# Optimization experiments

Hardware: AMD Instinct MI355X
Metric: run time of the kernel (lower is better)

## Reference

```python
import jax, jax.numpy as jnp
import numpy as np
import math

# static config (see shape_source)
NUM_GRAPHS = 8      # b
L_NODES = 1024      # nodes per graph (uniform -> to_dense_batch is a reshape)
D_INNER = 128
HEADDIM = 16
N_HEADS = D_INNER // HEADDIM  # 8
D_STATE = 64
NUM_DT = 4          # 3 node-dt components + dt_self
AVG_DEG = 16
DIAMETER = 50       # default_graph_diameter
TOL = 0.1
DT_MIN, DT_MAX, DT_FLOOR = 1e-3, 1e-1, 1e-4


def dag_inverse(A):
    """DAGInverse.forward: (I - A)^{-1} via repeated-squaring doubling.
    A: [b, h, l, l]. j = 2^ceil(log2(diameter)); out = prod (I + A^{2^k})."""
    j = 2 ** math.ceil(math.log2(DIAMETER))  # 64
    I = jnp.eye(A.shape[-1], dtype=A.dtype)
    last = A
    out = I + A
    for _ in range(2, int(math.log2(j)) + 1):  # 5 iterations
        last = last @ last
        out = out @ (I + last)
    return out


def setup_inputs() -> dict:
    key = jax.random.key(0)
    k = jax.random.split(key, 8)
    N = NUM_GRAPHS * L_NODES
    x = jax.random.normal(k[0], (N, D_INNER), jnp.float32)
    B_mat = jax.random.normal(k[1], (N, D_STATE), jnp.float32)
    C_mat = jax.random.normal(k[2], (N, D_STATE), jnp.float32)
    dt = jax.random.normal(k[3], (N, NUM_DT * N_HEADS), jnp.float32)
    # dt_bias init as in GraphSSD.__init__
    u = jax.random.uniform(k[4], (N_HEADS,), jnp.float32)
    dt0 = jnp.exp(u * (math.log(DT_MAX) - math.log(DT_MIN)) + math.log(DT_MIN))
    dt0 = jnp.clip(dt0, DT_FLOOR, None)
    dt_bias = dt0 + jnp.log(-jnp.expm1(-dt0))
    D = jnp.ones((N_HEADS,), jnp.float32)
    # edges: per-graph random endpoints, offset to global node ids
    E_per = L_NODES * AVG_DEG
    src_l = jax.random.randint(k[5], (NUM_GRAPHS, E_per), 0, L_NODES)
    dst_l = jax.random.randint(k[6], (NUM_GRAPHS, E_per), 0, L_NODES)
    off = (jnp.arange(NUM_GRAPHS) * L_NODES)[:, None]
    edge_index = jnp.stack([(src_l + off).reshape(-1), (dst_l + off).reshape(-1)], 0).astype(jnp.int32)
    return {"x": x, "B_mat": B_mat, "C_mat": C_mat, "dt": dt,
            "dt_bias": dt_bias, "D": D, "edge_index": edge_index}


def reference(x, B_mat, C_mat, dt, dt_bias, D, edge_index):
    Bn, Lg, H, hd, ds = NUM_GRAPHS, L_NODES, N_HEADS, HEADDIM, D_STATE
    N = Bn * Lg
    # dense batching (uniform graph sizes -> pure reshape, mask all True)
    x_d = x.reshape(Bn, Lg, H, hd).transpose(0, 2, 1, 3)        # b n l h ('(n h)' split)
    B_d = B_mat.reshape(Bn, Lg, ds)                             # broadcast over heads
    C_d = C_mat.reshape(Bn, Lg, ds)
    # dt: 'l (n c) -> c n l'
    dt_c = dt.reshape(N, H, NUM_DT).transpose(2, 1, 0)          # c n l
    dt_node, dt_self = dt_c[:NUM_DT - 1], dt_c[NUM_DT - 1]      # (3,n,N), (n,N)
    dt_self_d = dt_self.T.reshape(Bn, Lg, H).transpose(0, 2, 1)  # b n l
    # multiply_dt_w_A: A = -exp(A_log)= -1 (with_A=False)
    dt_A_node = -jax.nn.softplus(dt_node + dt_bias[None, :, None])  # (3, n, N)
    # edge dt: (dt_s[src] + dt_t[dst]) / 2, then exp
    src, dst = edge_index[0], edge_index[1]
    attr = jnp.exp((dt_A_node[0][:, src] + dt_A_node[1][:, dst]) * 0.5).T  # (E, n)
    # to_dense_adj scatter: [b, l1, l2, h] then -> b h l1 l2
    b_idx, sl, dl = src // Lg, src % Lg, dst % Lg
    A_mat = jnp.zeros((Bn, Lg, Lg, H), x.dtype).at[b_idx, sl, dl].add(attr)
    A_mat = A_mat.transpose(0, 3, 1, 2)                          # b n l1 l2
    # 'leq' normalization with dummy self term
    dt_dummy = jnp.exp(dt_A_node[2]).T.reshape(Bn, Lg, H).transpose(0, 2, 1)  # b n l
    normalizer = A_mat.sum(-1) + dt_dummy                        # b n l1
    A_norm = A_mat / (normalizer[..., None] + TOL)
    # L = (I - A^T)^{-1} via DAGInverse doubling
    Lmat = dag_inverse(jnp.swapaxes(A_norm, -1, -2).astype(jnp.float32))  # b n l t
    L_norm = Lmat * dt_self_d[:, :, None, :]                     # scale along t
    # y = einsum(C, L, B, x); C/B broadcast in heads -> G shared across heads
    G = jnp.einsum('bld,btd->blt', C_d, B_d)[:, None]            # b 1 l t
    y = jnp.einsum('bnlt,bnth->bnlh', L_norm * G, x_d)
    y = y + x_d * D[None, :, None, None]
    # 'b n l h -> b l (h n)'
    y = y.transpose(0, 2, 3, 1).reshape(Bn, Lg, H * hd)
    return y.reshape(N, H * hd)
```

## Files before the change

kernel.cpp:

```cpp
#include <hip/hip_runtime.h>
#include <hip/hip_bf16.h>

#define H_ 8
#define NTOT 8192
#define LG 1024
#define BN 8
#define HD 16
#define DSTATE 64
#define EPG 16384
#define MSZ (1024*1024)

typedef __hip_bfloat16 bf16;
typedef unsigned short ushort_t;
typedef _Float16 f16;
typedef __attribute__((ext_vector_type(8))) _Float16 half8;
typedef __attribute__((ext_vector_type(4))) _Float16 half4;
typedef __attribute__((ext_vector_type(4))) float f4v;

__device__ __forceinline__ float b2f(bf16 v){ return __bfloat162float(v); }
__device__ __forceinline__ float sp_(float z){
  return fmaxf(z, 0.f) + log1pf(expf(-fabsf(z)));
}
__device__ __forceinline__ float ldv(const void* p, size_t i, int f32){
  float v;
  if (f32) v = ((const float*)p)[i];
  else     v = b2f(((const bf16*)p)[i]);
  return v;
}
__device__ __forceinline__ void gl2lds16(const void* g, void* l){
  __builtin_amdgcn_global_load_lds((const __attribute__((address_space(1))) unsigned int*)g,
                                   (__attribute__((address_space(3))) unsigned int*)l,
                                   16, 0, 0);
}

__global__ void k_sniff(const void* __restrict__ dt, int* __restrict__ flag){
  const ushort_t* p = (const ushort_t*)dt;
  int tid = threadIdx.x;
  int bad = 0;
  for (int i = tid; i < 512; i += 256){
    int e = (p[i] >> 7) & 0xFF;
    if (e >= 140) bad = 1;
  }
  unsigned long long m = __ballot(bad != 0);
  __shared__ int anybad[4];
  if ((tid & 63) == 0) anybad[tid >> 6] = (m != 0ull) ? 1 : 0;
  __syncthreads();
  if (tid == 0) *flag = (anybad[0] | anybad[1] | anybad[2] | anybad[3]);
}

__global__ void k_nodecoef(const void* __restrict__ dt, const void* __restrict__ dtb,
                           const int* __restrict__ flag,
                           float* __restrict__ a0, float* __restrict__ a1,
                           float* __restrict__ dum, float* __restrict__ sdt){
  int idx = blockIdx.x*256 + threadIdx.x;
  if (idx >= H_*NTOT) return;
  int f32 = *flag;
  int h = idx / NTOT, n = idx - h*NTOT;
  float bias = ldv(dtb, h, f32);
  size_t base = (size_t)n*(4*H_) + h*4;
  float d0, d1, d2, d3;
  if (f32){
    const float* row = (const float*)dt + base;
    d0 = row[0]; d1 = row[1]; d2 = row[2]; d3 = row[3];
  } else {
    const bf16* row = (const bf16*)dt + base;
    d0 = b2f(row[0]); d1 = b2f(row[1]); d2 = b2f(row[2]); d3 = b2f(row[3]);
  }
  a0[idx]  = -sp_(d0 + bias);
  a1[idx]  = -sp_(d1 + bias);
  dum[idx] = expf(-sp_(d2 + bias));
  sdt[idx] = d3;
}

__global__ __launch_bounds__(256) void k_zero(char* base, size_t regB){
  int bh = blockIdx.y;
  float* Mf = (float*)(base + (size_t)bh*regB) + MSZ;
  int i = blockIdx.x*1024 + threadIdx.x*4;
  *(float4*)(Mf + i) = make_float4(0.f,0.f,0.f,0.f);
}

__global__ void k_scatter(const int* __restrict__ ei, const float* __restrict__ a0,
                          const float* __restrict__ a1, char* base, size_t regB,
                          float* __restrict__ nrm,
                          int b0, int h0, int lgHB, int GBp, int nthreads, int Etot){
  int t = blockIdx.x*256 + threadIdx.x;
  if (t >= nthreads) return;
  int HB = 1 << lgHB;
  int hl = t & (HB-1);
  int el = t >> lgHB;
  int e = b0*EPG + el;
  int src = ei[e], dst = ei[Etot + e];
  int g = src >> 10;
  if ((unsigned)(g - b0) >= (unsigned)GBp) return;
  int sl = src & 1023, dl = dst & 1023;
  int h = h0 + hl;
  float attr = expf(0.5f*(a0[h*NTOT + src] + a1[h*NTOT + dst]));
  int bhl = (g - b0)*HB + hl;
  float* Mf = (float*)(base + (size_t)bhl*regB) + MSZ;
  atomicAdd(&Mf[(size_t)dl*LG + sl], attr);
  atomicAdd(&nrm[bhl*LG + sl], attr);
}

__global__ void k_normalize(char* base, size_t regB,
                            const float* __restrict__ nrm, const float* __restrict__ dum,
                            int b0, int h0, int HB){
  size_t idx = (size_t)blockIdx.x*256 + threadIdx.x;
  int bh = (int)(idx >> 20);
  int rem = (int)(idx & (MSZ-1));
  int sl = rem & 1023, dl = rem >> 10;
  int g = b0 + bh / HB, h = h0 + bh % HB;
  const float* Mf = (const float*)(base + (size_t)bh*regB) + MSZ;
  f16* ub = (f16*)(base + (size_t)bh*regB);
  float denom = nrm[bh*LG + sl] + dum[h*NTOT + g*LG + sl] + 0.1f;
  float v = Mf[rem] / denom;
  ub[rem] = (f16)v;
  ub[(size_t)4*MSZ + rem] = (f16)(v + (dl == sl ? 1.f : 0.f));
}

__global__ __launch_bounds__(256) void k_transpose(char* base, size_t regB, int iS, int iD){
  __shared__ ushort_t t[32][33];
  int bh = blockIdx.z;
  const ushort_t* S = (const ushort_t*)(base + (size_t)bh*regB) + (size_t)iS*MSZ;
  ushort_t* D = (ushort_t*)(base + (size_t)bh*regB) + (size_t)iD*MSZ;
  int x0 = blockIdx.x*32, y0 = blockIdx.y*32;
  int tx = threadIdx.x & 31, ty = threadIdx.x >> 5;
  #pragma unroll
  for (int i = 0; i < 32; i += 8)
    t[ty+i][tx] = S[(size_t)(y0+ty+i)*LG + x0+tx];
  __syncthreads();
  #pragma unroll
  for (int i = 0; i < 32; i += 8)
    D[(size_t)(x0+ty+i)*LG + y0+tx] = t[tx][ty+i];
}

__global__ __launch_bounds__(256) void k_G(const void* __restrict__ Bm, const void* __restrict__ Cm,
                                           const int* __restrict__ flag,
                                           f16* __restrict__ G, int b0){
  int gl = blockIdx.z;
  int g = b0 + gl;
  int l0 = blockIdx.y*16, t0 = blockIdx.x*16;
  __shared__ float Cs[16][DSTATE+1];
  __shared__ float Bs[16][DSTATE+1];
  int tid = threadIdx.x;
  int f32 = *flag;
  if (f32){
    const float* Cf = (const float*)Cm;
    const float* Bf = (const float*)Bm;
    for (int i = tid; i < 16*DSTATE; i += 256){
      int r = i >> 6, d = i & 63;
      Cs[r][d] = Cf[(size_t)(g*LG + l0 + r)*DSTATE + d];
      Bs[r][d] = Bf[(size_t)(g*LG + t0 + r)*DSTATE + d];
    }
  } else {
    const bf16* Cb = (const bf16*)Cm;
    const bf16* Bb = (const bf16*)Bm;
    for (int i = tid; i < 16*DSTATE; i += 256){
      int r = i >> 6, d = i & 63;
      Cs[r][d] = b2f(Cb[(size_t)(g*LG + l0 + r)*DSTATE + d]);
      Bs[r][d] = b2f(Bb[(size_t)(g*LG + t0 + r)*DSTATE + d]);
    }
  }
  __syncthreads();
  int r = tid >> 4, c = tid & 15;
  float acc = 0.f;
  #pragma unroll
  for (int d = 0; d < DSTATE; ++d) acc = fmaf(Cs[r][d], Bs[c][d], acc);
  G[(size_t)gl*MSZ + (size_t)(l0+r)*LG + t0 + c] = (f16)acc;
}

__global__ __launch_bounds__(512, 6) void k_gemm_fused(char* base, size_t regB,
    int nS, int iAs, int iBTs, int iCs, int iCTs,
    int nU, int iAu, int iBTu, int iCu){
  __shared__ ushort_t As[2][4096];
  __shared__ ushort_t Bs[2][4096];
  int T = nS + nU;
  int s = blockIdx.x + 8*blockIdx.z;
  if (s >= T) return;
  int isS = (s < nS) ? 1 : 0;
  int bh  = isS ? s : (s - nS);
  int iA  = isS ? iAs : iAu;
  int iBT = isS ? iBTs : iBTu;
  int iC  = isS ? iCs : iCu;
  int iCT = isS ? iCTs : -1;
  int addA = 1 - isS;
  char* reg = base + (size_t)bh*regB;
  const f16* Ab = (const f16*)reg + (size_t)iA*MSZ;
  const f16* Bb = (const f16*)reg + (size_t)iBT*MSZ;
  f16* Cb = (f16*)reg + (size_t)iC*MSZ;
  int y = blockIdx.y;
  int i0 = (y >> 3)*128, j0 = (y & 7)*128;
  int tid = threadIdx.x;
  int lane = tid & 63, wv = tid >> 6;
  int wr = (wv >> 2)*64, wc = (wv & 3)*32;
  int m16 = lane & 15, q = lane >> 4;
  int srow = tid >> 2;
  int skq = (tid & 3) ^ ((tid >> 3) & 3);
  const f16* Ag = Ab + (size_t)(i0 + srow)*LG + skq*8;
  const f16* Bg = Bb + (size_t)(j0 + srow)*LG + skq*8;
  #define STAGE(K0, BUF) do { \
    gl2lds16(Ag + (K0), &As[BUF][(size_t)tid*8]); \
    gl2lds16(Bg + (K0), &Bs[BUF][(size_t)tid*8]); } while(0)
  STAGE(0, 0);
  f4v acc[4][2] = {};
  int slotq = q ^ ((m16 >> 1) & 3);
  int aoff = (wr + m16)*32 + slotq*8;
  int boff = (wc + m16)*32 + slotq*8;
  for (int k0 = 0; k0 < LG; k0 += 32){
    int cur = (k0 >> 5) & 1;
    __syncthreads();
    if (k0 + 32 < LG) STAGE(k0 + 32, cur ^ 1);
    half8 af[4], bfr[2];
    #pragma unroll
    for (int t = 0; t < 4; ++t)
      af[t]  = *(const half8*)&As[cur][aoff + t*512];
    #pragma unroll
    for (int t = 0; t < 2; ++t)
      bfr[t] = *(const half8*)&Bs[cur][boff + t*512];
    #pragma unroll
    for (int mt = 0; mt < 4; ++mt)
      #pragma unroll
      for (int nt = 0; nt < 2; ++nt)
        acc[mt][nt] = __builtin_amdgcn_mfma_f32_16x16x32_f16(af[mt], bfr[nt], acc[mt][nt], 0, 0, 0);
  }
  #undef STAGE
  f16* CT = (f16*)reg + (size_t)((iCT < 0) ? iC : iCT)*MSZ;
  #pragma unroll
  for (int mt = 0; mt < 4; ++mt){
    #pragma unroll
    for (int nt = 0; nt < 2; ++nt){
      int gr0 = i0 + wr + mt*16 + q*4;
      int gc = j0 + wc + nt*16 + m16;
      half4 tv;
      #pragma unroll
      for (int r = 0; r < 4; ++r){
        float v = acc[mt][nt][r];
        if (addA) v += (float)Ab[(size_t)(gr0 + r)*LG + gc];
        f16 hv = (f16)v;
        tv[r] = hv;
        Cb[(size_t)(gr0 + r)*LG + gc] = hv;
      }
      if (iCT >= 0)
        *(half4*)&CT[(size_t)gc*LG + gr0] = tv;
    }
  }
}

__global__ __launch_bounds__(256) void k_final2(char* base, size_t regB, int iO,
    const f16* __restrict__ Gh, const float* __restrict__ sdt,
    const void* __restrict__ x, const void* __restrict__ Dv,
    const int* __restrict__ flag, void* __restrict__ out,
    int b0, int h0, int HB){
  __shared__ float coef[16][257];
  int bh = blockIdx.y;
  int gl = bh / HB, g = b0 + gl, h = h0 + bh % HB;
  int L0r = blockIdx.x*16;
  int tid = threadIdx.x;
  int lr = tid >> 4, ts = tid & 15;
  int f32 = *flag;
  const f16* Orow = (const f16*)(base + (size_t)bh*regB) + (size_t)iO*MSZ + (size_t)(L0r+lr)*LG;
  const f16* Grow = Gh + (size_t)gl*MSZ + (size_t)(L0r+lr)*LG;
  const float* srow = sdt + h*NTOT + g*LG;
  float acc = 0.f;
  for (int tc = 0; tc < LG; tc += 256){
    int tb = tc + ts*16;
    __syncthreads();
    half8 o0 = *(const half8*)&Orow[tb];
    half8 o1 = *(const half8*)&Orow[tb + 8];
    half8 g0 = *(const half8*)&Grow[tb];
    half8 g1 = *(const half8*)&Grow[tb + 8];
    #pragma unroll
    for (int j = 0; j < 8; ++j){
      coef[lr][ts*16 + j]     = (float)o0[j] * (float)g0[j] * srow[tb + j];
      coef[lr][ts*16 + 8 + j] = (float)o1[j] * (float)g1[j] * srow[tb + 8 + j];
    }
    __syncthreads();
    if (f32){
      const float* xf = (const float*)x + (size_t)(g*LG + tc)*128 + h*HD + ts;
      for (int t = 0; t < 256; ++t)
        acc = fmaf(coef[lr][t], xf[(size_t)t*128], acc);
    } else {
      const bf16* xb = (const bf16*)x + (size_t)(g*LG + tc)*128 + h*HD + ts;
      for (int t = 0; t < 256; ++t)
        acc = fmaf(coef[lr][t], b2f(xb[(size_t)t*128]), acc);
    }
  }
  int l = L0r + lr, d = ts;
  float xs = ldv(x, (size_t)(g*LG + l)*128 + h*HD + d, f32);
  float dv = ldv(Dv, h, f32);
  float v = acc + xs*dv;
  size_t off = (size_t)(g*LG + l)*128 + d*H_ + h;
  if (f32) ((float*)out)[off] = v;
  else     ((bf16*)out)[off] = __float2bfloat16(v);
}

extern "C" void kernel_launch(void* const* d_in, const int* in_sizes, int n_in,
                              void* d_out, int out_size, void* d_ws, size_t ws_size,
                              hipStream_t stream){
  const void* x   = d_in[0];
  const void* Bm  = d_in[1];
  const void* Cm  = d_in[2];
  const void* dt  = d_in[3];
  const void* dtb = d_in[4];
  const void* Dv  = d_in[5];
  const int*  ei  = (const int*)d_in[6];
  int Etot = in_sizes[6] / 2;

  const size_t REG = (size_t)6*MSZ*2;
  int GB = 1, HB = 1;
  const int cfgs[7][2] = {{8,8},{4,8},{2,8},{1,8},{1,4},{1,2},{1,1}};
  for (int i = 0; i < 7; ++i){
    int gb = cfgs[i][0], hb = cfgs[i][1];
    size_t need = 4ull*(4ull*H_*NTOT + 64)
                + 4ull*(size_t)gb*hb*LG
                + 2ull*(size_t)gb*MSZ
                + (size_t)gb*hb*REG;
    if (need <= ws_size){ GB = gb; HB = hb; break; }
  }
  int lgHB = (HB==8)?3:((HB==4)?2:((HB==2)?1:0));
  int nbh = GB*HB;

  float* a0  = (float*)d_ws;
  float* a1  = a0 + H_*NTOT;
  float* dum = a1 + H_*NTOT;
  float* sdt = dum + H_*NTOT;
  int*  flag = (int*)(sdt + H_*NTOT);
  float* nrm = (float*)flag + 64;
  f16* G     = (f16*)(nrm + (size_t)nbh*LG);
  char* chainBase = (char*)(G + (size_t)GB*MSZ);

  k_sniff<<<1, 256, 0, stream>>>(dt, flag);
  k_nodecoef<<<(H_*NTOT + 255)/256, 256, 0, stream>>>(dt, dtb, flag, a0, a1, dum, sdt);

  for (int b0 = 0; b0 < BN; b0 += GB){
    for (int h0 = 0; h0 < H_; h0 += HB){
      k_zero<<<dim3(1024, nbh), 256, 0, stream>>>(chainBase, REG);
      (void)hipMemsetAsync(nrm, 0, (size_t)nbh*LG*sizeof(float), stream);
      int nthr = GB*EPG*HB;
      k_scatter<<<(nthr + 255)/256, 256, 0, stream>>>(ei, a0, a1, chainBase, REG, nrm,
                                                      b0, h0, lgHB, GB, nthr, Etot);
      k_normalize<<<nbh*(MSZ/256), 256, 0, stream>>>(chainBase, REG, nrm, dum, b0, h0, HB);
      k_transpose<<<dim3(32, 32, nbh), 256, 0, stream>>>(chainBase, REG, 0, 1);
      if (h0 == 0){
        dim3 gg(64, 64, GB);
        k_G<<<gg, 256, 0, stream>>>(Bm, Cm, flag, G, b0);
      }
      int lA = 0, lAT = 1, lC = 2, lCT = 3, oA = 4, oC = 5;
      {
        int T = nbh;
        dim3 gg(8, 64, (T + 7)/8);
        k_gemm_fused<<<gg, 512, 0, stream>>>(chainBase, REG, nbh, lA, lAT, lC, lCT,
                                             0, 0, 0, 0);
      }
      for (int k = 0; k < 4; ++k){
        int T = 2*nbh;
        dim3 gg(8, 64, (T + 7)/8);
        k_gemm_fused<<<gg, 512, 0, stream>>>(chainBase, REG,
                                             nbh, lC, lCT, lA, lAT,
                                             nbh, oA, lCT, oC);
        int tp;
        tp = lA; lA = lC; lC = tp;
        tp = lAT; lAT = lCT; lCT = tp;
        tp = oA; oA = oC; oC = tp;
      }
      {
        int T = nbh;
        dim3 gg(8, 64, (T + 7)/8);
        k_gemm_fused<<<gg, 512, 0, stream>>>(chainBase, REG, 0, 0, 0, 0, 0,
                                             nbh, oA, lCT, oC);
        int tp = oA; oA = oC; oC = tp;
      }
      dim3 fg(64, nbh);
      k_final2<<<fg, 256, 0, stream>>>(chainBase, REG, oA, G, sdt, x, Dv, flag, d_out, b0, h0, HB);
    }
  }
}
```

Before: 2.499 ms.

## Fuse normalize with transpose, split final reduction, fold nrm zeroing into k_zero

Merges the normalize and transpose kernels so the normalized fp16 matrix and its transpose are written in one pass, computing the reciprocal denominator once per column. Moves nrm zeroing into the zero kernel to drop a memset launch. Changes the a0/a1 layout to node-major so scatter reads for neighbouring heads are contiguous. Splits the final contraction over t into two halves written to scratch, with a new output kernel that sums them and adds the D skip term. This gives more blocks in the final stage at the cost of an extra launch and a scratch round-trip.

```diff
diff --git a/kernel.cpp b/kernel.cpp
--- a/kernel.cpp
+++ b/kernel.cpp
@@ -66,17 +66,22 @@
     const bf16* row = (const bf16*)dt + base;
     d0 = b2f(row[0]); d1 = b2f(row[1]); d2 = b2f(row[2]); d3 = b2f(row[3]);
   }
-  a0[idx]  = -sp_(d0 + bias);
-  a1[idx]  = -sp_(d1 + bias);
+  a0[(size_t)n*H_ + h] = -sp_(d0 + bias);
+  a1[(size_t)n*H_ + h] = -sp_(d1 + bias);
   dum[idx] = expf(-sp_(d2 + bias));
   sdt[idx] = d3;
 }
 
-__global__ __launch_bounds__(256) void k_zero(char* base, size_t regB){
+__global__ __launch_bounds__(256) void k_zero(char* base, size_t regB, float* __restrict__ nrm){
   int bh = blockIdx.y;
-  float* Mf = (float*)(base + (size_t)bh*regB) + MSZ;
-  int i = blockIdx.x*1024 + threadIdx.x*4;
-  *(float4*)(Mf + i) = make_float4(0.f,0.f,0.f,0.f);
+  if (blockIdx.x < 1024){
+    float* Mf = (float*)(base + (size_t)bh*regB) + MSZ;
+    int i = blockIdx.x*1024 + threadIdx.x*4;
+    *(float4*)(Mf + i) = make_float4(0.f,0.f,0.f,0.f);
+  } else {
+    int j = threadIdx.x*4;
+    *(float4*)(nrm + (size_t)bh*LG + j) = make_float4(0.f,0.f,0.f,0.f);
+  }
 }
 
 __global__ void k_scatter(const int* __restrict__ ei, const float* __restrict__ a0,
@@ -94,43 +99,44 @@
   if ((unsigned)(g - b0) >= (unsigned)GBp) return;
   int sl = src & 1023, dl = dst & 1023;
   int h = h0 + hl;
-  float attr = expf(0.5f*(a0[h*NTOT + src] + a1[h*NTOT + dst]));
+  float attr = expf(0.5f*(a0[(size_t)src*H_ + h] + a1[(size_t)dst*H_ + h]));
   int bhl = (g - b0)*HB + hl;
   float* Mf = (float*)(base + (size_t)bhl*regB) + MSZ;
   atomicAdd(&Mf[(size_t)dl*LG + sl], attr);
   atomicAdd(&nrm[bhl*LG + sl], attr);
 }
 
-__global__ void k_normalize(char* base, size_t regB,
+__global__ __launch_bounds__(256) void k_norm2(char* base, size_t regB,
                             const float* __restrict__ nrm, const float* __restrict__ dum,
                             int b0, int h0, int HB){
-  size_t idx = (size_t)blockIdx.x*256 + threadIdx.x;
-  int bh = (int)(idx >> 20);
-  int rem = (int)(idx & (MSZ-1));
-  int sl = rem & 1023, dl = rem >> 10;
+  __shared__ ushort_t tb[32][33];
+  int bh = blockIdx.z;
   int g = b0 + bh / HB, h = h0 + bh % HB;
   const float* Mf = (const float*)(base + (size_t)bh*regB) + MSZ;
-  f16* ub = (f16*)(base + (size_t)bh*regB);
-  float denom = nrm[bh*LG + sl] + dum[h*NTOT + g*LG + sl] + 0.1f;
-  float v = Mf[rem] / denom;
-  ub[rem] = (f16)v;
-  ub[(size_t)4*MSZ + rem] = (f16)(v + (dl == sl ? 1.f : 0.f));
-}
-
-__global__ __launch_bounds__(256) void k_transpose(char* base, size_t regB, int iS, int iD){
-  __shared__ ushort_t t[32][33];
-  int bh = blockIdx.z;
-  const ushort_t* S = (const ushort_t*)(base + (size_t)bh*regB) + (size_t)iS*MSZ;
-  ushort_t* D = (ushort_t*)(base + (size_t)bh*regB) + (size_t)iD*MSZ;
+  f16* L0  = (f16*)(base + (size_t)bh*regB);
+  f16* L0T = L0 + MSZ;
+  f16* O0  = L0 + (size_t)4*MSZ;
   int x0 = blockIdx.x*32, y0 = blockIdx.y*32;
   int tx = threadIdx.x & 31, ty = threadIdx.x >> 5;
+  int sl = x0 + tx;
+  float denom = nrm[(size_t)bh*LG + sl] + dum[(size_t)h*NTOT + g*LG + sl] + 0.1f;
+  float rden = 1.f / denom;
   #pragma unroll
-  for (int i = 0; i < 32; i += 8)
-    t[ty+i][tx] = S[(size_t)(y0+ty+i)*LG + x0+tx];
+  for (int i = 0; i < 32; i += 8){
+    int dl = y0 + ty + i;
+    float v = Mf[(size_t)dl*LG + sl] * rden;
+    f16 hv = (f16)v;
+    L0[(size_t)dl*LG + sl] = hv;
+    O0[(size_t)dl*LG + sl] = (f16)(v + (dl == sl ? 1.f : 0.f));
+    union { f16 h; ushort_t u; } cv; cv.h = hv;
+    tb[tx][ty + i] = cv.u;
+  }
   __syncthreads();
   #pragma unroll
-  for (int i = 0; i < 32; i += 8)
-    D[(size_t)(x0+ty+i)*LG + y0+tx] = t[tx][ty+i];
+  for (int i = 0; i < 32; i += 8){
+    union { f16 h; ushort_t u; } cv; cv.u = tb[ty + i][tx];
+    L0T[(size_t)(x0 + ty + i)*LG + y0 + tx] = cv.h;
+  }
 }
 
 __global__ __launch_bounds__(256) void k_G(const void* __restrict__ Bm, const void* __restrict__ Cm,
@@ -245,23 +251,26 @@
   }
 }
 
-__global__ __launch_bounds__(256) void k_final2(char* base, size_t regB, int iO,
+__global__ __launch_bounds__(256) void k_final3(char* base, size_t regB, int iO,
     const f16* __restrict__ Gh, const float* __restrict__ sdt,
-    const void* __restrict__ x, const void* __restrict__ Dv,
-    const int* __restrict__ flag, void* __restrict__ out,
+    const void* __restrict__ x, const int* __restrict__ flag,
     int b0, int h0, int HB){
   __shared__ float coef[16][257];
+  __shared__ float red[256];
   int bh = blockIdx.y;
   int gl = bh / HB, g = b0 + gl, h = h0 + bh % HB;
-  int L0r = blockIdx.x*16;
+  int lb = blockIdx.x >> 1, th = blockIdx.x & 1;
+  int L0r = lb*16;
   int tid = threadIdx.x;
   int lr = tid >> 4, ts = tid & 15;
   int f32 = *flag;
-  const f16* Orow = (const f16*)(base + (size_t)bh*regB) + (size_t)iO*MSZ + (size_t)(L0r+lr)*LG;
+  char* reg = base + (size_t)bh*regB;
+  const f16* Orow = (const f16*)reg + (size_t)iO*MSZ + (size_t)(L0r+lr)*LG;
   const f16* Grow = Gh + (size_t)gl*MSZ + (size_t)(L0r+lr)*LG;
-  const float* srow = sdt + h*NTOT + g*LG;
+  const float* srow = sdt + (size_t)h*NTOT + g*LG;
+  float* FS = (float*)reg;
   float acc = 0.f;
-  for (int tc = 0; tc < LG; tc += 256){
+  for (int tc = th*512; tc < th*512 + 512; tc += 256){
     int tb = tc + ts*16;
     __syncthreads();
     half8 o0 = *(const half8*)&Orow[tb];
@@ -284,10 +293,27 @@
         acc = fmaf(coef[lr][t], b2f(xb[(size_t)t*128]), acc);
     }
   }
-  int l = L0r + lr, d = ts;
+  red[tid] = acc;
+  __syncthreads();
+  FS[(size_t)th*16384 + (size_t)(L0r + lr)*16 + ts] = red[tid];
+}
+
+__global__ __launch_bounds__(256) void k_out(char* base, size_t regB,
+    const void* __restrict__ x, const void* __restrict__ Dv,
+    const int* __restrict__ flag, void* __restrict__ out,
+    int b0, int h0, int HB, int nbh){
+  int idx = blockIdx.x*256 + threadIdx.x;
+  if (idx >= nbh*LG*16) return;
+  int d = idx & 15;
+  int l = (idx >> 4) & 1023;
+  int bh = idx >> 14;
+  int g = b0 + bh / HB, h = h0 + bh % HB;
+  int f32 = *flag;
+  const float* FS = (const float*)(base + (size_t)bh*regB);
+  float v = FS[(size_t)l*16 + d] + FS[16384 + (size_t)l*16 + d];
   float xs = ldv(x, (size_t)(g*LG + l)*128 + h*HD + d, f32);
   float dv = ldv(Dv, h, f32);
-  float v = acc + xs*dv;
+  v += xs * dv;
   size_t off = (size_t)(g*LG + l)*128 + d*H_ + h;
   if (f32) ((float*)out)[off] = v;
   else     ((bf16*)out)[off] = __float2bfloat16(v);
@@ -333,13 +359,11 @@
 
   for (int b0 = 0; b0 < BN; b0 += GB){
     for (int h0 = 0; h0 < H_; h0 += HB){
-      k_zero<<<dim3(1024, nbh), 256, 0, stream>>>(chainBase, REG);
-      (void)hipMemsetAsync(nrm, 0, (size_t)nbh*LG*sizeof(float), stream);
+      k_zero<<<dim3(1025, nbh), 256, 0, stream>>>(chainBase, REG, nrm);
       int nthr = GB*EPG*HB;
       k_scatter<<<(nthr + 255)/256, 256, 0, stream>>>(ei, a0, a1, chainBase, REG, nrm,
                                                       b0, h0, lgHB, GB, nthr, Etot);
-      k_normalize<<<nbh*(MSZ/256), 256, 0, stream>>>(chainBase, REG, nrm, dum, b0, h0, HB);
-      k_transpose<<<dim3(32, 32, nbh), 256, 0, stream>>>(chainBase, REG, 0, 1);
+      k_norm2<<<dim3(32, 32, nbh), 256, 0, stream>>>(chainBase, REG, nrm, dum, b0, h0, HB);
       if (h0 == 0){
         dim3 gg(64, 64, GB);
         k_G<<<gg, 256, 0, stream>>>(Bm, Cm, flag, G, b0);
@@ -369,8 +393,11 @@
                                              nbh, oA, lCT, oC);
         int tp = oA; oA = oC; oC = tp;
       }
-      dim3 fg(64, nbh);
-      k_final2<<<fg, 256, 0, stream>>>(chainBase, REG, oA, G, sdt, x, Dv, flag, d_out, b0, h0, HB);
-    }
-  }
-}
+      dim3 fg(128, nbh);
+      k_final3<<<fg, 256, 0, stream>>>(chainBase, REG, oA, G, sdt, x, flag, b0, h0, HB);
+      int nout = nbh*LG*16;
+      k_out<<<(nout + 255)/256, 256, 0, stream>>>(chainBase, REG, x, Dv, flag, d_out,
+                                                  b0, h0, HB, nbh);
+    }
+  }
+}
```

Result: slower. 2.593 ms (+3.8%).
